# Kernel optimization log

Hardware: AMD Instinct MI355X
Metric: run time of the kernel (lower is better)

Reference implementation:

```python
import jax, jax.numpy as jnp
import numpy as np

NUM_EXPERTS = 64
INPUT_SIZE = 2048
NUM_TOKENS = 16384
TOPK = 8
INIT_STD = 0.02


def setup_inputs() -> dict:
    key = jax.random.key(0)
    k1, k2 = jax.random.split(key)
    input = jax.random.normal(k1, (NUM_TOKENS, INPUT_SIZE), dtype=jnp.float32)
    weight = INIT_STD * jax.random.normal(k2, (NUM_EXPERTS, INPUT_SIZE), dtype=jnp.float32)
    return {"input": input, "weight": weight}


def reference(input, weight):
    # gating GEMM: [N, D] x [E, D]^T -> [N, E]
    logits = jnp.einsum('nd,ed->ne', input, weight)
    n, e = logits.shape
    # pre_softmax=False branch: topk on raw logits, then softmax over selected
    top_scores, top_idx = jax.lax.top_k(logits, TOPK)          # [N, K]
    probs = jax.nn.softmax(top_scores.astype(jnp.float32), axis=-1).astype(logits.dtype)
    rows = jnp.arange(n)[:, None]                               # [N, 1]
    routing_probs = jnp.zeros_like(logits).at[rows, top_idx].set(probs)
    routing_map = jnp.zeros((n, e), dtype=jnp.bool_).at[rows, top_idx].set(True)
    return routing_probs, routing_map
```

## Files before the change

### kernel.cpp

```cpp
#include <hip/hip_runtime.h>
#include <cstdint>
#include <cmath>

#define D_DIM 2048
#define E_DIM 64
#define N_TOK 16384
#define K_TOP 8
#define KSTEP 32
#define KSLICE 4
#define TSTEPS 16
#define BLK_TOK 32
#define NFRAG 12

typedef __attribute__((ext_vector_type(8))) short bf16x8;
typedef __attribute__((ext_vector_type(4))) float f32x4;

union U4 { uint4 u; bf16x8 s; };

__device__ inline void split3_8(const float* a8, bf16x8& h, bf16x8& m, bf16x8& l) {
#pragma unroll
  for (int j = 0; j < 8; ++j) {
    const float x = a8[j];
    const unsigned u = __builtin_bit_cast(unsigned, x);
    const unsigned rh = (u + 0x7FFFu + ((u >> 16) & 1u)) & 0xFFFF0000u;
    h[j] = (short)(rh >> 16);
    const float r1 = x - __builtin_bit_cast(float, rh);
    const unsigned u1 = __builtin_bit_cast(unsigned, r1);
    const unsigned rm = (u1 + 0x7FFFu + ((u1 >> 16) & 1u)) & 0xFFFF0000u;
    m[j] = (short)(rm >> 16);
    const float r2 = r1 - __builtin_bit_cast(float, rm);
    l[j] = (short)(__builtin_bit_cast(unsigned, r2) >> 16);
  }
}

__global__ void wprep_kernel(const float* __restrict__ W, uint4* __restrict__ WF) {
  const int gid = blockIdx.x * 256 + threadIdx.x;
  const int lane = gid & 63;
  const int et = (gid >> 6) & 3;
  const int ks = gid >> 8;
  const int e = et * 16 + (lane & 15);
  const int kg = lane >> 4;
  const float* src = W + (size_t)e * D_DIM + ks * KSTEP + kg * 8;
  const float4 a = ((const float4*)src)[0];
  const float4 b = ((const float4*)src)[1];
  float a8[8] = {a.x, a.y, a.z, a.w, b.x, b.y, b.z, b.w};
  U4 h, m, l;
  split3_8(a8, h.s, m.s, l.s);
  const int fbase = (ks * NFRAG + et * 3) * 64 + lane;
  WF[fbase] = h.u;
  WF[fbase + 64] = m.u;
  WF[fbase + 128] = l.u;
}

#define BCV(x) __builtin_bit_cast(bf16x8, x)
#define MM(d, A, B) d = __builtin_amdgcn_mfma_f32_16x16x32_bf16(A, BCV(B), d, 0, 0, 0)

#define SPLIT3V(v0, v1, H, M, L)                                     \
  do {                                                               \
    float a8_[8] = {v0.x, v0.y, v0.z, v0.w, v1.x, v1.y, v1.z, v1.w}; \
    split3_8(a8_, H, M, L);                                          \
  } while (0)

__global__ __launch_bounds__(256, 2)
void gemm_router(const float* __restrict__ X, const uint4* __restrict__ WF,
                 float* __restrict__ Pout, float* __restrict__ Mout) {
  __shared__ float red[2][KSLICE][64][17];

  const int tid = threadIdx.x;
  const int w = tid >> 6;
  const int l = tid & 63;
  const int col = l & 15;
  const int kg = l >> 4;
  const int tok0 = blockIdx.x * BLK_TOK;

  const float* gX0 = X + (size_t)(tok0 + col) * D_DIM + w * (TSTEPS * KSTEP) + kg * 8;
  const float* gX1 = gX0 + (size_t)16 * D_DIM;
  const uint4* gB = WF + (size_t)w * TSTEPS * (NFRAG * 64) + l;

  f32x4 acc0[8], acc1[8];
#pragma unroll
  for (int i = 0; i < 8; ++i) { acc0[i] = (f32x4)0.f; acc1[i] = (f32x4)0.f; }

  float4 xa00, xa01, xa10, xa11;
  float4 xb00, xb01, xb10, xb11;
  uint4 bh[4], bm[4], bl[4];

#define LOAD_XA(t)                                    \
  do {                                                \
    const float* p0_ = gX0 + (t) * KSTEP;             \
    const float* p1_ = gX1 + (t) * KSTEP;             \
    xa00 = *(const float4*)p0_;                       \
    xa01 = *(const float4*)(p0_ + 4);                 \
    xa10 = *(const float4*)p1_;                       \
    xa11 = *(const float4*)(p1_ + 4);                 \
  } while (0)

#define LOAD_XB(t)                                    \
  do {                                                \
    const float* p0_ = gX0 + (t) * KSTEP;             \
    const float* p1_ = gX1 + (t) * KSTEP;             \
    xb00 = *(const float4*)p0_;                       \
    xb01 = *(const float4*)(p0_ + 4);                 \
    xb10 = *(const float4*)p1_;                       \
    xb11 = *(const float4*)(p1_ + 4);                 \
  } while (0)

#define LOAD_B(t)                                     \
  do {                                                \
    const uint4* bp_ = gB + (size_t)(t) * (NFRAG * 64); \
    bh[0] = bp_[0 * 64];  bm[0] = bp_[1 * 64];  bl[0] = bp_[2 * 64];  \
    bh[1] = bp_[3 * 64];  bm[1] = bp_[4 * 64];  bl[1] = bp_[5 * 64];  \
    bh[2] = bp_[6 * 64];  bm[2] = bp_[7 * 64];  bl[2] = bp_[8 * 64];  \
    bh[3] = bp_[9 * 64];  bm[3] = bp_[10 * 64]; bl[3] = bp_[11 * 64]; \
  } while (0)

#define CRUNCH(AH0, AM0, AL0, AH1, AM1, AL1)                               \
  do {                                                                     \
    _Pragma("unroll") for (int et = 0; et < 4; ++et) MM(acc0[et], AH0, bh[et]);      \
    _Pragma("unroll") for (int et = 0; et < 4; ++et) MM(acc0[4 + et], AH1, bh[et]);  \
    _Pragma("unroll") for (int et = 0; et < 4; ++et) MM(acc1[et], AH0, bm[et]);      \
    _Pragma("unroll") for (int et = 0; et < 4; ++et) MM(acc1[4 + et], AH1, bm[et]);  \
    _Pragma("unroll") for (int et = 0; et < 4; ++et) MM(acc1[et], AM0, bh[et]);      \
    _Pragma("unroll") for (int et = 0; et < 4; ++et) MM(acc1[4 + et], AM1, bh[et]);  \
    _Pragma("unroll") for (int et = 0; et < 4; ++et) MM(acc1[et], AH0, bl[et]);      \
    _Pragma("unroll") for (int et = 0; et < 4; ++et) MM(acc1[4 + et], AH1, bl[et]);  \
    _Pragma("unroll") for (int et = 0; et < 4; ++et) MM(acc1[et], AL0, bh[et]);      \
    _Pragma("unroll") for (int et = 0; et < 4; ++et) MM(acc1[4 + et], AL1, bh[et]);  \
    _Pragma("unroll") for (int et = 0; et < 4; ++et) MM(acc1[et], AM0, bm[et]);      \
    _Pragma("unroll") for (int et = 0; et < 4; ++et) MM(acc1[4 + et], AM1, bm[et]);  \
  } while (0)

  LOAD_XA(0);
  LOAD_XB(1);

#pragma unroll 1
  for (int t = 0; t < TSTEPS; t += 2) {
    {
      LOAD_B(t);
      bf16x8 ah0, am0, al0, ah1, am1, al1;
      SPLIT3V(xa00, xa01, ah0, am0, al0);
      SPLIT3V(xa10, xa11, ah1, am1, al1);
      if (t + 2 < TSTEPS) LOAD_XA(t + 2);
      CRUNCH(ah0, am0, al0, ah1, am1, al1);
    }
    {
      LOAD_B(t + 1);
      bf16x8 ah0, am0, al0, ah1, am1, al1;
      SPLIT3V(xb00, xb01, ah0, am0, al0);
      SPLIT3V(xb10, xb11, ah1, am1, al1);
      if (t + 3 < TSTEPS) LOAD_XB(t + 3);
      CRUNCH(ah0, am0, al0, ah1, am1, al1);
    }
  }

#pragma unroll
  for (int mt = 0; mt < 2; ++mt)
#pragma unroll
    for (int et = 0; et < 4; ++et)
#pragma unroll
      for (int q = 0; q < 4; ++q)
        red[mt][w][l][et * 4 + q] = acc0[mt * 4 + et][q] + acc1[mt * 4 + et][q];

  __syncthreads();
  if (w >= 2) return;

  float fin[16];
#pragma unroll
  for (int i = 0; i < 16; ++i) {
    float s = red[w][0][l][i];
    s += red[w][1][l][i];
    s += red[w][2][l][i];
    s += red[w][3][l][i];
    fin[i] = s;
  }

#pragma unroll
  for (int q = 0; q < 4; ++q) {
    float v[4];
#pragma unroll
    for (int et = 0; et < 4; ++et) v[et] = fin[et * 4 + q];

    float topv[K_TOP];
    int topi[K_TOP];
#pragma unroll
    for (int t = 0; t < K_TOP; ++t) {
      float bv = v[0];
      int bi = col;
#pragma unroll
      for (int et = 1; et < 4; ++et) {
        const bool take = v[et] > bv;
        bv = take ? v[et] : bv;
        bi = take ? (et * 16 + col) : bi;
      }
#pragma unroll
      for (int off = 1; off < 16; off <<= 1) {
        const float ov = __shfl_xor(bv, off, 64);
        const int oi = __shfl_xor(bi, off, 64);
        const bool take = (ov > bv) || (ov == bv && oi < bi);
        bv = take ? ov : bv;
        bi = take ? oi : bi;
      }
      topv[t] = bv;
      topi[t] = bi;
#pragma unroll
      for (int et = 0; et < 4; ++et)
        if (bi == et * 16 + col) v[et] = -INFINITY;
    }

    float p[K_TOP], sum = 0.f;
#pragma unroll
    for (int t = 0; t < K_TOP; ++t) {
      p[t] = expf(topv[t] - topv[0]);
      sum += p[t];
    }
    const float inv = 1.f / sum;

    const int tok = tok0 + w * 16 + kg * 4 + q;
#pragma unroll
    for (int et = 0; et < 4; ++et) {
      const int e = et * 16 + col;
      float pv = 0.f, mv = 0.f;
#pragma unroll
      for (int t = 0; t < K_TOP; ++t) {
        const bool hit = (topi[t] == e);
        pv = hit ? p[t] * inv : pv;
        mv = hit ? 1.f : mv;
      }
      Pout[(size_t)tok * E_DIM + e] = pv;
      Mout[(size_t)tok * E_DIM + e] = mv;
    }
  }
}

extern "C" void kernel_launch(void* const* d_in, const int* in_sizes, int n_in,
                              void* d_out, int out_size, void* d_ws, size_t ws_size,
                              hipStream_t stream) {
  const float* X = (const float*)d_in[0];
  const float* W = (const float*)d_in[1];
  float* P = (float*)d_out;
  float* M = P + (size_t)N_TOK * E_DIM;
  uint4* WF = (uint4*)d_ws;

  wprep_kernel<<<dim3(64), dim3(256), 0, stream>>>(W, WF);
  gemm_router<<<dim3(N_TOK / BLK_TOK), dim3(256), 0, stream>>>(X, WF, P, M);
}
```

Baseline: 55.25 us.

## Split K-slice GEMM into single-wave blocks with global partials and separate top-k reduce

Replaces the 256-thread block that reduced four K-slices through shared memory with 2048 single-wave blocks, each computing one K-slice partial for 32 tokens and writing it to a workspace buffer. A new reduce kernel sums the four partials and does top-k with a wave-wide max and ballot, then the softmax. The inner loop is restructured into half-B-fragment stages with sched_barriers so loads overlap the MFMAs. This adds a 16 MB partial write and read plus an extra launch in exchange for finer-grained scheduling and more occupancy. The old fused kernel is kept as a fallback when the workspace is too small.

```diff
diff --git a/kernel.cpp b/kernel.cpp
--- a/kernel.cpp
+++ b/kernel.cpp
@@ -7,9 +7,7 @@
 #define N_TOK 16384
 #define K_TOP 8
 #define KSTEP 32
-#define KSLICE 4
 #define TSTEPS 16
-#define BLK_TOK 32
 #define NFRAG 12
 
 typedef __attribute__((ext_vector_type(8))) short bf16x8;
@@ -61,17 +59,174 @@
     split3_8(a8_, H, M, L);                                          \
   } while (0)
 
+
+__global__ __launch_bounds__(64, 3)
+void gemm_partial(const float* __restrict__ X, const uint4* __restrict__ WF,
+                  float* __restrict__ Part) {
+  const int bid = blockIdx.x;
+  const int ks = bid & 3;
+  const int mt = bid >> 2;
+  const int l = threadIdx.x;
+  const int col = l & 15;
+  const int kg = l >> 4;
+  const int tok0 = mt * 32;
+
+  const float* gX0 = X + (size_t)(tok0 + col) * D_DIM + ks * (TSTEPS * KSTEP) + kg * 8;
+  const float* gX1 = gX0 + (size_t)16 * D_DIM;
+  const uint4* gB = WF + (size_t)ks * TSTEPS * (NFRAG * 64) + l;
+
+  f32x4 acc0[8], acc1[8];
+#pragma unroll
+  for (int i = 0; i < 8; ++i) { acc0[i] = (f32x4)0.f; acc1[i] = (f32x4)0.f; }
+
+  float4 x00, x01, x10, x11;
+  uint4 bA[6], bB[6];
+
+#define LOAD_X(t)                         \
+  do {                                    \
+    const float* p0_ = gX0 + (t) * KSTEP; \
+    const float* p1_ = gX1 + (t) * KSTEP; \
+    x00 = *(const float4*)p0_;            \
+    x01 = *(const float4*)(p0_ + 4);      \
+    x10 = *(const float4*)p1_;            \
+    x11 = *(const float4*)(p1_ + 4);      \
+  } while (0)
+
+#define LOAD_BA(t)                                      \
+  do {                                                  \
+    const uint4* bp_ = gB + (size_t)(t) * (NFRAG * 64); \
+    bA[0] = bp_[0 * 64]; bA[1] = bp_[1 * 64];           \
+    bA[2] = bp_[2 * 64]; bA[3] = bp_[3 * 64];           \
+    bA[4] = bp_[4 * 64]; bA[5] = bp_[5 * 64];           \
+  } while (0)
+
+#define LOAD_BB(t)                                      \
+  do {                                                  \
+    const uint4* bp_ = gB + (size_t)(t) * (NFRAG * 64); \
+    bB[0] = bp_[6 * 64];  bB[1] = bp_[7 * 64];          \
+    bB[2] = bp_[8 * 64];  bB[3] = bp_[9 * 64];          \
+    bB[4] = bp_[10 * 64]; bB[5] = bp_[11 * 64];         \
+  } while (0)
+
+#define CRUNCH_HALF(BARR, BASE, AH0, AM0, AL0, AH1, AM1, AL1)          \
+  do {                                                                 \
+    _Pragma("unroll") for (int e2 = 0; e2 < 2; ++e2) {                 \
+      MM(acc0[BASE + e2], AH0, BARR[e2 * 3]);                          \
+      MM(acc0[4 + BASE + e2], AH1, BARR[e2 * 3]);                      \
+    }                                                                  \
+    _Pragma("unroll") for (int e2 = 0; e2 < 2; ++e2) {                 \
+      MM(acc1[BASE + e2], AH0, BARR[e2 * 3 + 1]);                      \
+      MM(acc1[4 + BASE + e2], AH1, BARR[e2 * 3 + 1]);                  \
+    }                                                                  \
+    _Pragma("unroll") for (int e2 = 0; e2 < 2; ++e2) {                 \
+      MM(acc1[BASE + e2], AM0, BARR[e2 * 3]);                          \
+      MM(acc1[4 + BASE + e2], AM1, BARR[e2 * 3]);                      \
+    }                                                                  \
+    _Pragma("unroll") for (int e2 = 0; e2 < 2; ++e2) {                 \
+      MM(acc1[BASE + e2], AH0, BARR[e2 * 3 + 2]);                      \
+      MM(acc1[4 + BASE + e2], AH1, BARR[e2 * 3 + 2]);                  \
+    }                                                                  \
+    _Pragma("unroll") for (int e2 = 0; e2 < 2; ++e2) {                 \
+      MM(acc1[BASE + e2], AL0, BARR[e2 * 3]);                          \
+      MM(acc1[4 + BASE + e2], AL1, BARR[e2 * 3]);                      \
+    }                                                                  \
+    _Pragma("unroll") for (int e2 = 0; e2 < 2; ++e2) {                 \
+      MM(acc1[BASE + e2], AM0, BARR[e2 * 3 + 1]);                      \
+      MM(acc1[4 + BASE + e2], AM1, BARR[e2 * 3 + 1]);                  \
+    }                                                                  \
+  } while (0)
+
+  LOAD_X(0);
+  LOAD_BA(0);
+  LOAD_BB(0);
+
+#pragma unroll 1
+  for (int t = 0; t < TSTEPS; ++t) {
+    bf16x8 ah0, am0, al0, ah1, am1, al1;
+    SPLIT3V(x00, x01, ah0, am0, al0);
+    SPLIT3V(x10, x11, ah1, am1, al1);
+    if (t + 1 < TSTEPS) LOAD_X(t + 1);
+    __builtin_amdgcn_sched_barrier(0);
+    CRUNCH_HALF(bA, 0, ah0, am0, al0, ah1, am1, al1);
+    if (t + 1 < TSTEPS) LOAD_BA(t + 1);
+    __builtin_amdgcn_sched_barrier(0);
+    CRUNCH_HALF(bB, 2, ah0, am0, al0, ah1, am1, al1);
+    if (t + 1 < TSTEPS) LOAD_BB(t + 1);
+    __builtin_amdgcn_sched_barrier(0);
+  }
+
+#pragma unroll
+  for (int mt2 = 0; mt2 < 2; ++mt2)
+#pragma unroll
+    for (int q = 0; q < 4; ++q) {
+      const int tok = tok0 + mt2 * 16 + kg * 4 + q;
+      float* dst = Part + ((size_t)ks * N_TOK + tok) * E_DIM + col;
+#pragma unroll
+      for (int et = 0; et < 4; ++et)
+        dst[et * 16] = acc0[mt2 * 4 + et][q] + acc1[mt2 * 4 + et][q];
+    }
+}
+
+__global__ __launch_bounds__(256)
+void reduce_router(const float* __restrict__ Part,
+                   float* __restrict__ Pout, float* __restrict__ Mout) {
+  const int lane = threadIdx.x & 63;
+  const int gw = blockIdx.x * 4 + (threadIdx.x >> 6);
+
+#pragma unroll 1
+  for (int j = 0; j < 8; ++j) {
+    const int tok = gw * 8 + j;
+    const size_t base = (size_t)tok * E_DIM + lane;
+    float v = Part[base];
+    v += Part[(size_t)1 * N_TOK * E_DIM + base];
+    v += Part[(size_t)2 * N_TOK * E_DIM + base];
+    v += Part[(size_t)3 * N_TOK * E_DIM + base];
+
+    float topv[K_TOP];
+    int topi[K_TOP];
+#pragma unroll
+    for (int kk = 0; kk < K_TOP; ++kk) {
+      float m = v;
+#pragma unroll
+      for (int off = 32; off > 0; off >>= 1)
+        m = fmaxf(m, __shfl_xor(m, off, 64));
+      const unsigned long long bal = __ballot(v == m);
+      const int li = __ffsll(bal) - 1;
+      topv[kk] = m;
+      topi[kk] = li;
+      if (lane == li) v = -INFINITY;
+    }
+
+    float p[K_TOP], sum = 0.f;
+#pragma unroll
+    for (int kk = 0; kk < K_TOP; ++kk) {
+      p[kk] = expf(topv[kk] - topv[0]);
+      sum += p[kk];
+    }
+    const float inv = 1.f / sum;
+
+    float pv = 0.f, mv = 0.f;
+#pragma unroll
+    for (int kk = 0; kk < K_TOP; ++kk)
+      if (topi[kk] == lane) { pv = p[kk] * inv; mv = 1.f; }
+
+    Pout[(size_t)tok * E_DIM + lane] = pv;
+    Mout[(size_t)tok * E_DIM + lane] = mv;
+  }
+}
+
+
 __global__ __launch_bounds__(256, 2)
-void gemm_router(const float* __restrict__ X, const uint4* __restrict__ WF,
-                 float* __restrict__ Pout, float* __restrict__ Mout) {
-  __shared__ float red[2][KSLICE][64][17];
+void gemm_router_fb(const float* __restrict__ X, const uint4* __restrict__ WF,
+                    float* __restrict__ Pout, float* __restrict__ Mout) {
+  __shared__ float red[2][4][64][17];
 
   const int tid = threadIdx.x;
   const int w = tid >> 6;
   const int l = tid & 63;
   const int col = l & 15;
   const int kg = l >> 4;
-  const int tok0 = blockIdx.x * BLK_TOK;
+  const int tok0 = blockIdx.x * 32;
 
   const float* gX0 = X + (size_t)(tok0 + col) * D_DIM + w * (TSTEPS * KSTEP) + kg * 8;
   const float* gX1 = gX0 + (size_t)16 * D_DIM;
@@ -81,85 +236,35 @@
 #pragma unroll
   for (int i = 0; i < 8; ++i) { acc0[i] = (f32x4)0.f; acc1[i] = (f32x4)0.f; }
 
-  float4 xa00, xa01, xa10, xa11;
-  float4 xb00, xb01, xb10, xb11;
-  uint4 bh[4], bm[4], bl[4];
-
-#define LOAD_XA(t)                                    \
-  do {                                                \
-    const float* p0_ = gX0 + (t) * KSTEP;             \
-    const float* p1_ = gX1 + (t) * KSTEP;             \
-    xa00 = *(const float4*)p0_;                       \
-    xa01 = *(const float4*)(p0_ + 4);                 \
-    xa10 = *(const float4*)p1_;                       \
-    xa11 = *(const float4*)(p1_ + 4);                 \
-  } while (0)
-
-#define LOAD_XB(t)                                    \
-  do {                                                \
-    const float* p0_ = gX0 + (t) * KSTEP;             \
-    const float* p1_ = gX1 + (t) * KSTEP;             \
-    xb00 = *(const float4*)p0_;                       \
-    xb01 = *(const float4*)(p0_ + 4);                 \
-    xb10 = *(const float4*)p1_;                       \
-    xb11 = *(const float4*)(p1_ + 4);                 \
-  } while (0)
-
-#define LOAD_B(t)                                     \
-  do {                                                \
-    const uint4* bp_ = gB + (size_t)(t) * (NFRAG * 64); \
-    bh[0] = bp_[0 * 64];  bm[0] = bp_[1 * 64];  bl[0] = bp_[2 * 64];  \
-    bh[1] = bp_[3 * 64];  bm[1] = bp_[4 * 64];  bl[1] = bp_[5 * 64];  \
-    bh[2] = bp_[6 * 64];  bm[2] = bp_[7 * 64];  bl[2] = bp_[8 * 64];  \
-    bh[3] = bp_[9 * 64];  bm[3] = bp_[10 * 64]; bl[3] = bp_[11 * 64]; \
-  } while (0)
-
-#define CRUNCH(AH0, AM0, AL0, AH1, AM1, AL1)                               \
-  do {                                                                     \
-    _Pragma("unroll") for (int et = 0; et < 4; ++et) MM(acc0[et], AH0, bh[et]);      \
-    _Pragma("unroll") for (int et = 0; et < 4; ++et) MM(acc0[4 + et], AH1, bh[et]);  \
-    _Pragma("unroll") for (int et = 0; et < 4; ++et) MM(acc1[et], AH0, bm[et]);      \
-    _Pragma("unroll") for (int et = 0; et < 4; ++et) MM(acc1[4 + et], AH1, bm[et]);  \
-    _Pragma("unroll") for (int et = 0; et < 4; ++et) MM(acc1[et], AM0, bh[et]);      \
-    _Pragma("unroll") for (int et = 0; et < 4; ++et) MM(acc1[4 + et], AM1, bh[et]);  \
-    _Pragma("unroll") for (int et = 0; et < 4; ++et) MM(acc1[et], AH0, bl[et]);      \
-    _Pragma("unroll") for (int et = 0; et < 4; ++et) MM(acc1[4 + et], AH1, bl[et]);  \
-    _Pragma("unroll") for (int et = 0; et < 4; ++et) MM(acc1[et], AL0, bh[et]);      \
-    _Pragma("unroll") for (int et = 0; et < 4; ++et) MM(acc1[4 + et], AL1, bh[et]);  \
-    _Pragma("unroll") for (int et = 0; et < 4; ++et) MM(acc1[et], AM0, bm[et]);      \
-    _Pragma("unroll") for (int et = 0; et < 4; ++et) MM(acc1[4 + et], AM1, bm[et]);  \
-  } while (0)
-
-  LOAD_XA(0);
-  LOAD_XB(1);
+  float4 x00, x01, x10, x11;
+  uint4 bA[6], bB[6];
+
+  LOAD_X(0);
+  LOAD_BA(0);
+  LOAD_BB(0);
 
 #pragma unroll 1
-  for (int t = 0; t < TSTEPS; t += 2) {
-    {
-      LOAD_B(t);
-      bf16x8 ah0, am0, al0, ah1, am1, al1;
-      SPLIT3V(xa00, xa01, ah0, am0, al0);
-      SPLIT3V(xa10, xa11, ah1, am1, al1);
-      if (t + 2 < TSTEPS) LOAD_XA(t + 2);
-      CRUNCH(ah0, am0, al0, ah1, am1, al1);
-    }
-    {
-      LOAD_B(t + 1);
-      bf16x8 ah0, am0, al0, ah1, am1, al1;
-      SPLIT3V(xb00, xb01, ah0, am0, al0);
-      SPLIT3V(xb10, xb11, ah1, am1, al1);
-      if (t + 3 < TSTEPS) LOAD_XB(t + 3);
-      CRUNCH(ah0, am0, al0, ah1, am1, al1);
-    }
-  }
-
-#pragma unroll
-  for (int mt = 0; mt < 2; ++mt)
+  for (int t = 0; t < TSTEPS; ++t) {
+    bf16x8 ah0, am0, al0, ah1, am1, al1;
+    SPLIT3V(x00, x01, ah0, am0, al0);
+    SPLIT3V(x10, x11, ah1, am1, al1);
+    if (t + 1 < TSTEPS) LOAD_X(t + 1);
+    __builtin_amdgcn_sched_barrier(0);
+    CRUNCH_HALF(bA, 0, ah0, am0, al0, ah1, am1, al1);
+    if (t + 1 < TSTEPS) LOAD_BA(t + 1);
+    __builtin_amdgcn_sched_barrier(0);
+    CRUNCH_HALF(bB, 2, ah0, am0, al0, ah1, am1, al1);
+    if (t + 1 < TSTEPS) LOAD_BB(t + 1);
+    __builtin_amdgcn_sched_barrier(0);
+  }
+
+#pragma unroll
+  for (int mt2 = 0; mt2 < 2; ++mt2)
 #pragma unroll
     for (int et = 0; et < 4; ++et)
 #pragma unroll
       for (int q = 0; q < 4; ++q)
-        red[mt][w][l][et * 4 + q] = acc0[mt * 4 + et][q] + acc1[mt * 4 + et][q];
+        red[mt2][w][l][et * 4 + q] = acc0[mt2 * 4 + et][q] + acc1[mt2 * 4 + et][q];
 
   __syncthreads();
   if (w >= 2) return;
@@ -239,8 +344,16 @@
   const float* W = (const float*)d_in[1];
   float* P = (float*)d_out;
   float* M = P + (size_t)N_TOK * E_DIM;
+
   uint4* WF = (uint4*)d_ws;
+  float* Part = (float*)((char*)d_ws + (size_t)(1 << 20));
+  const size_t needed = (size_t)(1 << 20) + (size_t)4 * N_TOK * E_DIM * sizeof(float);
 
   wprep_kernel<<<dim3(64), dim3(256), 0, stream>>>(W, WF);
-  gemm_router<<<dim3(N_TOK / BLK_TOK), dim3(256), 0, stream>>>(X, WF, P, M);
-}
+  if (ws_size >= needed) {
+    gemm_partial<<<dim3(2048), dim3(64), 0, stream>>>(X, WF, Part);
+    reduce_router<<<dim3(512), dim3(256), 0, stream>>>(Part, P, M);
+  } else {
+    gemm_router_fb<<<dim3(512), dim3(256), 0, stream>>>(X, WF, P, M);
+  }
+}
```

Result: slower. 76.47 us (+38.4%).
